# Optimization experiments

Hardware: AMD Instinct MI355X
Metric: run time of the kernel (lower is better)

## Reference

```python
import jax, jax.numpy as jnp
import numpy as np

N = 100000      # n_entities + n_users (graph nodes)
E = 1600000     # edges
R = 8           # relations
D = 64          # entity_dim
DR = 64         # relation_dim
EPS = 1e-12


def setup_inputs() -> dict:
    key = jax.random.key(0)
    ks = jax.random.split(key, 16)
    inp = {
        'entity_emb': jax.random.normal(ks[0], (N, D), jnp.float32) * 0.1,
        'rel_emb':    jax.random.normal(ks[1], (R, DR), jnp.float32) * 0.1,
        'W_R':        jax.random.normal(ks[2], (R, D, DR), jnp.float32) * 0.1,
        'W1_0': jax.random.normal(ks[3], (32, 64), jnp.float32) * 0.1,
        'b1_0': jax.random.normal(ks[4], (32,), jnp.float32) * 0.1,
        'W2_0': jax.random.normal(ks[5], (32, 64), jnp.float32) * 0.1,
        'b2_0': jax.random.normal(ks[6], (32,), jnp.float32) * 0.1,
        'W1_1': jax.random.normal(ks[7], (16, 32), jnp.float32) * 0.1,
        'b1_1': jax.random.normal(ks[8], (16,), jnp.float32) * 0.1,
        'W2_1': jax.random.normal(ks[9], (16, 32), jnp.float32) * 0.1,
        'b2_1': jax.random.normal(ks[10], (16,), jnp.float32) * 0.1,
        'src':   jax.random.randint(ks[11], (E,), 0, N, dtype=jnp.int32),
        'dst':   jax.random.randint(ks[12], (E,), 0, N, dtype=jnp.int32),
        'etype': jax.random.randint(ks[13], (E,), 0, R, dtype=jnp.int32),
    }
    return inp


def _l2_normalize(x):
    # F.normalize(x, p=2, dim=1)
    n = jnp.linalg.norm(x, axis=1, keepdims=True)
    return x / jnp.maximum(n, EPS)


def reference(entity_emb, rel_emb, W_R, W1_0, b1_0, W2_0, b2_0,
              W1_1, b1_1, W2_1, b2_1, src, dst, etype):
    # ---- compute_attention: per-edge relation-specific projection ----
    # proj[n, r, :] = entity_emb[n] @ W_R[r]   -> [N, R, DR]
    proj = jnp.einsum('nd,rdk->nrk', entity_emb, W_R)
    r_mul_t = proj[src, etype]          # [E, DR] (edges.src)
    r_mul_h = proj[dst, etype]          # [E, DR] (edges.dst)
    r_e = rel_emb[etype]                # [E, DR]
    att = jnp.sum(r_mul_t * jnp.tanh(r_mul_h + r_e), axis=-1)  # [E]

    # ---- edge_softmax: normalize over incoming edges of each dst ----
    m = jax.ops.segment_max(att, dst, num_segments=N)           # [N]
    ex = jnp.exp(att - m[dst])
    s = jax.ops.segment_sum(ex, dst, num_segments=N)            # [N]
    a = ex / s[dst]                                             # [E]

    # ---- bi-interaction aggregator layers ----
    def agg_layer(x, W1, b1, W2, b2):
        msg = x[src] * a[:, None]                               # u_mul_e
        Nh = jax.ops.segment_sum(msg, dst, num_segments=N)      # sum to dst
        out1 = jax.nn.leaky_relu(jnp.matmul(x + Nh, W1.T) + b1, 0.01)
        out2 = jax.nn.leaky_relu(jnp.matmul(x * Nh, W2.T) + b2, 0.01)
        return _l2_normalize(out1 + out2)

    ego = entity_emb
    h1 = agg_layer(ego, W1_0, b1_0, W2_0, b2_0)   # [N, 32]
    h2 = agg_layer(h1, W1_1, b1_1, W2_1, b2_1)    # [N, 16]
    all_embed = jnp.concatenate([ego, h1, h2], axis=1)  # [N, 112]
    return all_embed
```

## Files before the change

kernel.cpp:

```cpp
#include <hip/hip_runtime.h>
#include <hip/hip_bf16.h>
#include <math.h>

#define NN 100000
#define NE 1600000
#define NR 8
#define DD 64
#define DDR 64

typedef __attribute__((ext_vector_type(8))) short bf8v;
typedef __attribute__((ext_vector_type(4))) float f4v;

__device__ __forceinline__ unsigned enc_f(float f) {
    unsigned u = __float_as_uint(f);
    return (u & 0x80000000u) ? ~u : (u | 0x80000000u);
}
__device__ __forceinline__ float dec_f(unsigned u) {
    return (u & 0x80000000u) ? __uint_as_float(u & 0x7FFFFFFFu) : __uint_as_float(~u);
}
__device__ __forceinline__ float bflo(unsigned u) { return __uint_as_float(u << 16); }
__device__ __forceinline__ float bfhi(unsigned u) { return __uint_as_float(u & 0xFFFF0000u); }
__device__ __forceinline__ float bfs2f(unsigned short u) { return __uint_as_float(((unsigned)u) << 16); }
__device__ __forceinline__ short f2bfs(float x) {
    __hip_bfloat16 h = __float2bfloat16(x);
    return *reinterpret_cast<short*>(&h);
}
__device__ __forceinline__ unsigned pack2bf(short a, short b) {
    return (unsigned)(unsigned short)a | ((unsigned)(unsigned short)b << 16);
}
__device__ __forceinline__ float tanh_fast(float x) {
    x = fminf(fmaxf(x, -15.f), 15.f);
    float e = __expf(2.f * x);
    return (e - 1.f) * __builtin_amdgcn_rcpf(e + 1.f);
}

__global__ void __launch_bounds__(256)
k_projf(const float* __restrict__ emb, const float* __restrict__ WR,
        const float* __restrict__ rel,
        unsigned short* __restrict__ w2h, unsigned* __restrict__ embh)
{
    __shared__ unsigned short Tt[128][66];
    int t = threadIdx.x;
    int wv = t >> 6, l = t & 63;
    int lo = l & 15, hi = l >> 4;
    int r = blockIdx.y;
    int colbase = (wv & 1) * 32;
    int p = wv >> 1;
    int nwbase = blockIdx.x * 128 + p * 64;
    int nlocal = p * 64;

    const float* __restrict__ wb = WR + (long)r * (DD * DDR) + (hi * 8) * DDR + colbase + lo;
    {
        bf8v B00, B01, B10, B11;
#pragma unroll
        for (int j = 0; j < 8; ++j) {
            B00[j] = f2bfs(wb[(0 * 32 + j) * DDR + 0]);
            B01[j] = f2bfs(wb[(1 * 32 + j) * DDR + 0]);
            B10[j] = f2bfs(wb[(0 * 32 + j) * DDR + 16]);
            B11[j] = f2bfs(wb[(1 * 32 + j) * DDR + 16]);
        }
        float rv0 = rel[r * DDR + colbase + lo];
        float rv1 = rel[r * DDR + colbase + lo + 16];

        for (int nt = 0; nt < 4; ++nt) {
            int nb = nwbase + nt * 16;
            int arow = nb + lo;
            float4 xa0 = make_float4(0.f, 0.f, 0.f, 0.f), xa1 = xa0, xb0 = xa0, xb1 = xa0;
            if (arow < NN) {
                const float* __restrict__ xr = emb + (long)arow * DD + hi * 8;
                xa0 = *(const float4*)(xr);
                xa1 = *(const float4*)(xr + 4);
                xb0 = *(const float4*)(xr + 32);
                xb1 = *(const float4*)(xr + 36);
            }
            bf8v A0, A1;
            A0[0] = f2bfs(xa0.x); A0[1] = f2bfs(xa0.y); A0[2] = f2bfs(xa0.z); A0[3] = f2bfs(xa0.w);
            A0[4] = f2bfs(xa1.x); A0[5] = f2bfs(xa1.y); A0[6] = f2bfs(xa1.z); A0[7] = f2bfs(xa1.w);
            A1[0] = f2bfs(xb0.x); A1[1] = f2bfs(xb0.y); A1[2] = f2bfs(xb0.z); A1[3] = f2bfs(xb0.w);
            A1[4] = f2bfs(xb1.x); A1[5] = f2bfs(xb1.y); A1[6] = f2bfs(xb1.z); A1[7] = f2bfs(xb1.w);

            if (r == 0 && arow < NN) {
                unsigned* er = embh + (long)arow * 32 + hi * 4;
                er[0]  = pack2bf(A0[0], A0[1]); er[1]  = pack2bf(A0[2], A0[3]);
                er[2]  = pack2bf(A0[4], A0[5]); er[3]  = pack2bf(A0[6], A0[7]);
                er[16] = pack2bf(A1[0], A1[1]); er[17] = pack2bf(A1[2], A1[3]);
                er[18] = pack2bf(A1[4], A1[5]); er[19] = pack2bf(A1[6], A1[7]);
            }

            f4v acc0 = {0.f, 0.f, 0.f, 0.f}, acc1 = {0.f, 0.f, 0.f, 0.f};
            acc0 = __builtin_amdgcn_mfma_f32_16x16x32_bf16(A0, B00, acc0, 0, 0, 0);
            acc0 = __builtin_amdgcn_mfma_f32_16x16x32_bf16(A1, B01, acc0, 0, 0, 0);
            acc1 = __builtin_amdgcn_mfma_f32_16x16x32_bf16(A0, B10, acc1, 0, 0, 0);
            acc1 = __builtin_amdgcn_mfma_f32_16x16x32_bf16(A1, B11, acc1, 0, 0, 0);

#pragma unroll
            for (int i = 0; i < 4; ++i) {
                int rl = nlocal + nt * 16 + hi * 4 + i;
                Tt[rl][colbase + lo]      = (unsigned short)f2bfs(tanh_fast(acc0[i] + rv0));
                Tt[rl][colbase + lo + 16] = (unsigned short)f2bfs(tanh_fast(acc1[i] + rv1));
            }
        }
    }
    __syncthreads();

    const float* __restrict__ wb0 = WR + (long)r * (DD * DDR) + (long)(colbase + lo) * DDR + hi * 8;
    const float* __restrict__ wb1 = wb0 + 16 * DDR;
    bf8v C00, C01, C10, C11;
#pragma unroll
    for (int j = 0; j < 8; ++j) {
        C00[j] = f2bfs(wb0[j]);
        C01[j] = f2bfs(wb0[32 + j]);
        C10[j] = f2bfs(wb1[j]);
        C11[j] = f2bfs(wb1[32 + j]);
    }
    for (int nt = 0; nt < 4; ++nt) {
        int nb = nwbase + nt * 16;
        int rl = nlocal + nt * 16 + lo;
        bf8v A0 = *(const bf8v*)&Tt[rl][hi * 8];
        bf8v A1 = *(const bf8v*)&Tt[rl][32 + hi * 8];
        f4v acc0 = {0.f, 0.f, 0.f, 0.f}, acc1 = {0.f, 0.f, 0.f, 0.f};
        acc0 = __builtin_amdgcn_mfma_f32_16x16x32_bf16(A0, C00, acc0, 0, 0, 0);
        acc0 = __builtin_amdgcn_mfma_f32_16x16x32_bf16(A1, C01, acc0, 0, 0, 0);
        acc1 = __builtin_amdgcn_mfma_f32_16x16x32_bf16(A0, C10, acc1, 0, 0, 0);
        acc1 = __builtin_amdgcn_mfma_f32_16x16x32_bf16(A1, C11, acc1, 0, 0, 0);
#pragma unroll
        for (int i = 0; i < 4; ++i) {
            int rr = nb + hi * 4 + i;
            if (rr < NN) {
                long obase = ((long)r * NN + rr) * DDR + colbase + lo;
                w2h[obase]      = (unsigned short)f2bfs(acc0[i]);
                w2h[obase + 16] = (unsigned short)f2bfs(acc1[i]);
            }
        }
    }
}

__global__ void k_hist(const int* __restrict__ dst, unsigned* __restrict__ cnt)
{
    int e = blockIdx.x * blockDim.x + threadIdx.x;
    if (e >= NE) return;
    atomicAdd(cnt + dst[e], 1u);
}

__global__ void k_base(const unsigned* __restrict__ cnt, unsigned* __restrict__ gcur,
                       unsigned* __restrict__ base, unsigned* __restrict__ curs)
{
    int i = blockIdx.x * blockDim.x + threadIdx.x;
    int lane = threadIdx.x & 63;
    unsigned v = (i < NN) ? cnt[i] : 0u;
    unsigned p = v;
#pragma unroll
    for (int off = 1; off < 64; off <<= 1) {
        unsigned q = __shfl_up(p, off);
        if (lane >= off) p += q;
    }
    unsigned tot = __shfl(p, 63);
    unsigned gb = 0;
    if (lane == 0) gb = atomicAdd(gcur, tot);
    gb = __shfl(gb, 0);
    if (i < NN) {
        unsigned b = gb + p - v;
        base[i] = b;
        curs[i] = b;
    }
}

__global__ void k_scatter2(const int* __restrict__ dst, const int* __restrict__ src,
                           const int* __restrict__ et, unsigned* __restrict__ curs,
                           unsigned* __restrict__ srcet)
{
    int e = blockIdx.x * blockDim.x + threadIdx.x;
    if (e >= NE) return;
    unsigned pos = atomicAdd(curs + dst[e], 1u);
    srcet[pos] = (unsigned)src[e] | ((unsigned)et[e] << 28);
}

__global__ void __launch_bounds__(256)
k_mega0(const float* __restrict__ emb, const unsigned* __restrict__ embh,
        const unsigned* __restrict__ w2h,
        const unsigned* __restrict__ cnt, const unsigned* __restrict__ basep,
        const unsigned* __restrict__ srcet, float* __restrict__ acsr,
        unsigned short* __restrict__ h1h,
        const float* __restrict__ W1, const float* __restrict__ b1,
        const float* __restrict__ W2, const float* __restrict__ b2,
        float* __restrict__ out)
{
    __shared__ float W1T[64][33];
    __shared__ float W2T[64][33];
    __shared__ float sm1[4][64];
    __shared__ float sm2[4][64];
    int t = threadIdx.x;
#pragma unroll
    for (int i = 0; i < 8; ++i) {
        int idx = i * 256 + t;
        W1T[idx & 63][idx >> 6] = W1[idx];
        W2T[idx & 63][idx >> 6] = W2[idx];
    }
    int wv = t >> 6, lane = t & 63;
    int g = blockIdx.x * 4 + wv;
    int deg = (int)cnt[g];
    long b = basep[g];
    float Nh = 0.f;
    const unsigned short* embh_us = (const unsigned short*)embh;
    if (deg > 0 && deg <= 64) {
        unsigned se = 0;
        if (lane < deg) se = srcet[b + lane];
        int gi = lane >> 4;
        int lj = lane & 15;
        float acc = 0.f, s_ = 0.f, myexp = 0.f;
        for (int k0 = 0; k0 < deg; k0 += 4) {
            int ei = k0 + gi;
            unsigned sei = __shfl(se, ei);
            int s = (int)(sei & 0x0FFFFFFFu);
            int r = (int)(sei >> 28);
            uint2 tv = *(const uint2*)(embh + (long)s * 32 + lj * 2);
            uint2 hv = *(const uint2*)(w2h + ((long)r * NN + g) * 32 + lj * 2);
            float sum = bflo(tv.x) * bflo(hv.x) + bfhi(tv.x) * bfhi(hv.x)
                      + bflo(tv.y) * bflo(hv.y) + bfhi(tv.y) * bfhi(hv.y);
#pragma unroll
            for (int off = 8; off; off >>= 1) sum += __shfl_xor(sum, off);
#pragma unroll
            for (int q = 0; q < 4; ++q) {
                float sq = __shfl(sum, q * 16);
                float exq = (k0 + q < deg) ? __expf(fminf(sq, 60.f)) : 0.f;
                if (lane == k0 + q) myexp = exq;
                s_ += exq;
                int srcl = q * 16 + (lane >> 2);
                unsigned rx = __shfl(tv.x, srcl);
                unsigned ry = __shfl(tv.y, srcl);
                unsigned word = (lane & 2) ? ry : rx;
                float v = (lane & 1) ? bfhi(word) : bflo(word);
                acc = fmaf(v, exq, acc);
            }
        }
        float inv = 1.f / s_;
        if (lane < deg) acsr[b + lane] = myexp * inv;
        Nh = acc * inv;
    } else if (deg > 64) {
        float m = -3.4e38f;
        for (int i = 0; i < deg; ++i) {
            unsigned sei = srcet[b + i];
            int s = (int)(sei & 0x0FFFFFFFu), r = (int)(sei >> 28);
            float v = bfs2f(embh_us[(long)s * DD + lane]);
            float wvl = bfs2f(((const unsigned short*)w2h)[((long)r * NN + g) * DDR + lane]);
            float p = v * wvl;
#pragma unroll
            for (int off = 32; off; off >>= 1) p += __shfl_xor(p, off);
            if (lane == 0) acsr[b + i] = p;
            m = fmaxf(m, p);
        }
        float s_ = 0.f;
        for (int i = lane; i < deg; i += 64) s_ += __expf(acsr[b + i] - m);
#pragma unroll
        for (int off = 32; off; off >>= 1) s_ += __shfl_xor(s_, off);
        float inv = 1.f / s_;
        float acc = 0.f;
        for (int i = 0; i < deg; ++i) {
            float raw = acsr[b + i];
            float a = __expf(raw - m) * inv;
            int s = (int)(srcet[b + i] & 0x0FFFFFFFu);
            acc = fmaf(bfs2f(embh_us[(long)s * DD + lane]), a, acc);
            if (lane == 0) acsr[b + i] = a;
        }
        Nh = acc;
    }
    float x = emb[(long)g * DD + lane];
    sm1[wv][lane] = x + Nh;
    sm2[wv][lane] = x * Nh;
    __syncthreads();
    int j = lane & 31;
    const float* __restrict__ WT = (lane < 32) ? &W1T[0][0] : &W2T[0][0];
    const float* __restrict__ sm = (lane < 32) ? &sm1[wv][0] : &sm2[wv][0];
    float accm = (lane < 32) ? b1[j] : b2[j];
#pragma unroll 8
    for (int dd = 0; dd < 64; ++dd)
        accm = fmaf(sm[dd], WT[dd * 33 + j], accm);
    accm = (accm >= 0.f) ? accm : 0.01f * accm;
    float other = __shfl_down(accm, 32);
    float h = accm + other;
    float ss = h * h;
#pragma unroll
    for (int off = 16; off; off >>= 1) ss += __shfl_xor(ss, off);
    float hn = h / fmaxf(sqrtf(ss), 1e-12f);
    out[(long)g * 112 + lane] = x;
    if (lane < 32) {
        out[(long)g * 112 + 64 + j] = hn;
        h1h[(long)g * 32 + j] = (unsigned short)f2bfs(hn);
    }
}

__global__ void __launch_bounds__(256)
k_mega1(const float* __restrict__ acsr, const unsigned* __restrict__ srcet,
        const unsigned* __restrict__ cnt, const unsigned* __restrict__ basep,
        const unsigned short* __restrict__ h1h,
        const float* __restrict__ W1, const float* __restrict__ b1,
        const float* __restrict__ W2, const float* __restrict__ b2,
        float* __restrict__ out)
{
    __shared__ float W1T[32][17];
    __shared__ float W2T[32][17];
    __shared__ float sm1[8][32];
    __shared__ float sm2[8][32];
    int t = threadIdx.x;
#pragma unroll
    for (int i = 0; i < 2; ++i) {
        int idx = i * 256 + t;
        W1T[idx & 31][idx >> 5] = W1[idx];
        W2T[idx & 31][idx >> 5] = W2[idx];
    }
    int grp = t >> 5, l5 = t & 31;
    int g = blockIdx.x * 8 + grp;
    int deg = (int)cnt[g];
    float acc = 0.f;
    if (deg > 0) {
        long b = basep[g];
        unsigned se = 0; float a = 0.f;
        if (l5 < deg) { se = srcet[b + l5]; a = acsr[b + l5]; }
        int dmin = (deg < 32) ? deg : 32;
        int i = 0;
        for (; i + 1 < dmin; i += 2) {
            float a0 = __shfl(a, i, 32), a1 = __shfl(a, i + 1, 32);
            int s0 = (int)(__shfl(se, i, 32) & 0x0FFFFFFFu);
            int s1 = (int)(__shfl(se, i + 1, 32) & 0x0FFFFFFFu);
            float v0 = bfs2f(h1h[(long)s0 * 32 + l5]);
            float v1 = bfs2f(h1h[(long)s1 * 32 + l5]);
            acc = fmaf(v0, a0, acc);
            acc = fmaf(v1, a1, acc);
        }
        if (i < dmin) {
            float a0 = __shfl(a, i, 32);
            int s0 = (int)(__shfl(se, i, 32) & 0x0FFFFFFFu);
            acc = fmaf(bfs2f(h1h[(long)s0 * 32 + l5]), a0, acc);
        }
        for (int k = 32; k < deg; ++k) {
            float ak = acsr[b + k];
            int sk = (int)(srcet[b + k] & 0x0FFFFFFFu);
            acc = fmaf(bfs2f(h1h[(long)sk * 32 + l5]), ak, acc);
        }
    }
    float x = out[(long)g * 112 + 64 + l5];
    sm1[grp][l5] = x + acc;
    sm2[grp][l5] = x * acc;
    __syncthreads();
    int j = l5 & 15;
    const float* __restrict__ WT = (l5 < 16) ? &W1T[0][0] : &W2T[0][0];
    const float* __restrict__ sm = (l5 < 16) ? &sm1[grp][0] : &sm2[grp][0];
    float accm = (l5 < 16) ? b1[j] : b2[j];
#pragma unroll 8
    for (int dd = 0; dd < 32; ++dd)
        accm = fmaf(sm[dd], WT[dd * 17 + j], accm);
    accm = (accm >= 0.f) ? accm : 0.01f * accm;
    float other = __shfl_down(accm, 16, 32);
    float h = accm + other;
    float ss = h * h;
#pragma unroll
    for (int off = 8; off; off >>= 1) ss += __shfl_xor(ss, off);
    float hn = h / fmaxf(sqrtf(ss), 1e-12f);
    if (l5 < 16) out[(long)g * 112 + 96 + j] = hn;
}

__global__ void k_att(const float* __restrict__ emb, const float* __restrict__ rel,
                      const float* __restrict__ WR, const int* __restrict__ src,
                      const int* __restrict__ dst, const int* __restrict__ et,
                      float* __restrict__ att, unsigned* __restrict__ mkey)
{
    int e = (int)((blockIdx.x * blockDim.x + threadIdx.x) >> 6);
    int lane = threadIdx.x & 63;
    if (e >= NE) return;
    int s = src[e], d = dst[e], r = et[e];
    const float* __restrict__ es = emb + (long)s * DD;
    const float* __restrict__ eh = emb + (long)d * DD;
    const float* __restrict__ w  = WR + r * (DD * DDR) + lane;
    float at = 0.f, ah = 0.f;
#pragma unroll 8
    for (int dd = 0; dd < DD; ++dd) {
        float ws = w[dd * DDR];
        at = fmaf(es[dd], ws, at);
        ah = fmaf(eh[dd], ws, ah);
    }
    float term = at * tanhf(ah + rel[r * DDR + lane]);
#pragma unroll
    for (int off = 32; off; off >>= 1) term += __shfl_xor(term, off);
    if (lane == 0) {
        att[e] = term;
        atomicMax(mkey + d, enc_f(term));
    }
}

__global__ void k_expsum(const int* __restrict__ dst, float* __restrict__ att,
                         const unsigned* __restrict__ mkey, float* __restrict__ ssum)
{
    int e = blockIdx.x * blockDim.x + threadIdx.x;
    if (e >= NE) return;
    int d = dst[e];
    float ex = expf(att[e] - dec_f(mkey[d]));
    att[e] = ex;
    atomicAdd(ssum + d, ex);
}

__global__ void k_agg0(const float* __restrict__ emb, const int* __restrict__ src,
                       const int* __restrict__ dst, float* __restrict__ att,
                       const float* __restrict__ ssum, float* __restrict__ Nh)
{
    int e = (int)((blockIdx.x * blockDim.x + threadIdx.x) >> 6);
    int lane = threadIdx.x & 63;
    if (e >= NE) return;
    int s = src[e], d = dst[e];
    float a = att[e] / ssum[d];
    if (lane == 0) att[e] = a;
    float v = emb[(long)s * DD + lane] * a;
    atomicAdd(Nh + (long)d * DD + lane, v);
}

__global__ void k_agg1(const float* __restrict__ out, const int* __restrict__ src,
                       const int* __restrict__ dst, const float* __restrict__ att,
                       float* __restrict__ Nh1)
{
    int idx = blockIdx.x * blockDim.x + threadIdx.x;
    int e = idx >> 5;
    int j = idx & 31;
    if (e >= NE) return;
    int s = src[e], d = dst[e];
    float a = att[e];
    float v = out[(long)s * 112 + 64 + j] * a;
    atomicAdd(Nh1 + (long)d * 32 + j, v);
}

#define NPB0 32
__global__ void __launch_bounds__(256)
k_node0t(const float* __restrict__ emb, const float* __restrict__ Nh,
         const float* __restrict__ W1, const float* __restrict__ b1,
         const float* __restrict__ W2, const float* __restrict__ b2,
         float* __restrict__ out)
{
    __shared__ float W1T[64][33];
    __shared__ float W2T[64][33];
    int t = threadIdx.x;
#pragma unroll
    for (int i = 0; i < 8; ++i) {
        int idx = i * 256 + t;
        W1T[idx & 63][idx >> 6] = W1[idx];
        W2T[idx & 63][idx >> 6] = W2[idx];
    }
    __syncthreads();
    int wv = t >> 6, lane = t & 63, j = lane & 31;
    const float* __restrict__ WT = (lane < 32) ? &W1T[0][0] : &W2T[0][0];
    float bj = (lane < 32) ? b1[j] : b2[j];
    int n0 = blockIdx.x * NPB0;
    int n1 = (n0 + NPB0 < NN) ? n0 + NPB0 : NN;
    for (int node = n0 + wv; node < n1; node += 4) {
        const float* __restrict__ x  = emb + (long)node * DD;
        const float* __restrict__ nh = Nh + (long)node * DD;
        float acc = 0.f;
#pragma unroll 8
        for (int dd = 0; dd < DD; ++dd) {
            float xv = x[dd], nv = nh[dd];
            float v = (lane < 32) ? (xv + nv) : (xv * nv);
            acc = fmaf(v, WT[dd * 33 + j], acc);
        }
        acc += bj;
        acc = (acc >= 0.f) ? acc : 0.01f * acc;
        float other = __shfl_down(acc, 32);
        float h = acc + other;
        float ss = h * h;
#pragma unroll
        for (int off = 16; off; off >>= 1) ss += __shfl_xor(ss, off);
        float hn = h / fmaxf(sqrtf(ss), 1e-12f);
        out[(long)node * 112 + lane] = x[lane];
        if (lane < 32) out[(long)node * 112 + 64 + j] = hn;
    }
}

#define NPB1 32
__global__ void __launch_bounds__(256)
k_node1t(const float* __restrict__ outbuf, const float* __restrict__ Nh1,
         const float* __restrict__ W1, const float* __restrict__ b1,
         const float* __restrict__ W2, const float* __restrict__ b2,
         float* __restrict__ out)
{
    __shared__ float W1T[32][17];
    __shared__ float W2T[32][17];
    int t = threadIdx.x;
#pragma unroll
    for (int i = 0; i < 2; ++i) {
        int idx = i * 256 + t;
        W1T[idx & 31][idx >> 5] = W1[idx];
        W2T[idx & 31][idx >> 5] = W2[idx];
    }
    __syncthreads();
    int grp = t >> 5;
    int l5 = t & 31, j = l5 & 15;
    const float* __restrict__ WT = (l5 < 16) ? &W1T[0][0] : &W2T[0][0];
    float bj = (l5 < 16) ? b1[j] : b2[j];
    int n0 = blockIdx.x * NPB1;
    int n1 = (n0 + NPB1 < NN) ? n0 + NPB1 : NN;
    for (int node = n0 + grp; node < n1; node += 8) {
        const float* __restrict__ x  = outbuf + (long)node * 112 + 64;
        const float* __restrict__ nh = Nh1 + (long)node * 32;
        float acc = 0.f;
#pragma unroll 8
        for (int dd = 0; dd < 32; ++dd) {
            float xv = x[dd], nv = nh[dd];
            float v = (l5 < 16) ? (xv + nv) : (xv * nv);
            acc = fmaf(v, WT[dd * 17 + j], acc);
        }
        acc += bj;
        acc = (acc >= 0.f) ? acc : 0.01f * acc;
        float other = __shfl_down(acc, 16, 32);
        float h = acc + other;
        float ss = h * h;
#pragma unroll
        for (int off = 8; off; off >>= 1) ss += __shfl_xor(ss, off);
        float hn = h / fmaxf(sqrtf(ss), 1e-12f);
        if (l5 < 16) out[(long)node * 112 + 96 + j] = hn;
    }
}

extern "C" void kernel_launch(void* const* d_in, const int* in_sizes, int n_in,
                              void* d_out, int out_size, void* d_ws, size_t ws_size,
                              hipStream_t stream) {
    const float* emb  = (const float*)d_in[0];
    const float* rel  = (const float*)d_in[1];
    const float* WR   = (const float*)d_in[2];
    const float* W1_0 = (const float*)d_in[3];
    const float* b1_0 = (const float*)d_in[4];
    const float* W2_0 = (const float*)d_in[5];
    const float* b2_0 = (const float*)d_in[6];
    const float* W1_1 = (const float*)d_in[7];
    const float* b1_1 = (const float*)d_in[8];
    const float* W2_1 = (const float*)d_in[9];
    const float* b2_1 = (const float*)d_in[10];
    const int*   src  = (const int*)d_in[11];
    const int*   dst  = (const int*)d_in[12];
    const int*   et   = (const int*)d_in[13];
    float* out = (float*)d_out;

    unsigned* cnt   = (unsigned*)d_ws;
    unsigned* gcur  = cnt + NN;
    unsigned* basep = cnt + NN + 64;
    unsigned* curs  = cnt + 2 * NN + 64;
    float* acsr  = (float*)d_ws + 3 * NN + 64;
    unsigned* srcet = (unsigned*)(acsr + NE);
    unsigned short* w2h = (unsigned short*)(srcet + NE);
    unsigned* embh = (unsigned*)(w2h + (size_t)NR * NN * DDR);
    unsigned short* h1h = (unsigned short*)(embh + (size_t)NN * 32);

    size_t need = ((size_t)3 * NN + 64 + 2 * (size_t)NE) * 4
                + (size_t)NR * NN * DDR * 2
                + (size_t)NN * 32 * 4 + (size_t)NN * 16 * 4;

    if (ws_size >= need) {
        hipMemsetAsync(d_ws, 0, (size_t)(NN + 64) * sizeof(unsigned), stream);
        k_hist<<<dim3((NE + 255) / 256), dim3(256), 0, stream>>>(dst, cnt);
        k_projf<<<dim3((NN + 127) / 128, NR), dim3(256), 0, stream>>>(
            emb, WR, rel, w2h, embh);
        k_base<<<dim3((NN + 255) / 256), dim3(256), 0, stream>>>(cnt, gcur, basep, curs);
        k_scatter2<<<dim3((NE + 255) / 256), dim3(256), 0, stream>>>(
            dst, src, et, curs, srcet);
        k_mega0<<<dim3((NN + 3) / 4), dim3(256), 0, stream>>>(
            emb, embh, (const unsigned*)w2h, cnt, basep, srcet, acsr, h1h,
            W1_0, b1_0, W2_0, b2_0, out);
        k_mega1<<<dim3((NN + 7) / 8), dim3(256), 0, stream>>>(
            acsr, srcet, cnt, basep, h1h, W1_1, b1_1, W2_1, b2_1, out);
    } else {
        unsigned* mkey = (unsigned*)d_ws;
        float* ssum = (float*)d_ws + NN;
        float* fNh0 = (float*)d_ws + 2 * NN;
        float* fNh1 = (float*)d_ws + (2 + DD) * NN;
        float* fatt = (float*)d_ws + (2 + DD + 32) * NN;
        hipMemsetAsync(d_ws, 0, (size_t)(2 + DD + 32) * NN * sizeof(float), stream);
        k_att<<<dim3((int)(((long)NE * 64 + 255) / 256)), dim3(256), 0, stream>>>(
            emb, rel, WR, src, dst, et, fatt, mkey);
        k_expsum<<<dim3((NE + 255) / 256), dim3(256), 0, stream>>>(dst, fatt, mkey, ssum);
        k_agg0<<<dim3((int)(((long)NE * 64 + 255) / 256)), dim3(256), 0, stream>>>(
            emb, src, dst, fatt, ssum, fNh0);
        k_node0t<<<dim3((NN + NPB0 - 1) / NPB0), dim3(256), 0, stream>>>(
            emb, fNh0, W1_0, b1_0, W2_0, b2_0, out);
        k_agg1<<<dim3((int)(((long)NE * 32 + 255) / 256)), dim3(256), 0, stream>>>(
            out, src, dst, fatt, fNh1);
        k_node1t<<<dim3((NN + NPB1 - 1) / NPB1), dim3(256), 0, stream>>>(
            out, fNh1, W1_1, b1_1, W2_1, b2_1, out);
    }
}
```

Before: 484.6 us.

## Loop over relations inside projection kernel to reuse loaded embedding rows

The projection kernel now gives each block 64 nodes and loops over all 8 relations inside the block, instead of launching one block per (128-node tile, relation). Each embedding row is loaded from global memory and converted to bf16 once, then reused for every relation, rather than being reread 8 times. The trade-off is that W_R is reloaded for every relation in every block, and two block-wide barriers are added per relation. The grid drops from 782x8 blocks to 1563, so each block does more sequential work.

After: 498.7 us. 2.9% more time.

```diff
diff --git a/kernel.cpp b/kernel.cpp
--- a/kernel.cpp
+++ b/kernel.cpp
@@ -35,103 +35,108 @@
 }
 
 __global__ void __launch_bounds__(256)
-k_projf(const float* __restrict__ emb, const float* __restrict__ WR,
-        const float* __restrict__ rel,
-        unsigned short* __restrict__ w2h, unsigned* __restrict__ embh)
-{
-    __shared__ unsigned short Tt[128][66];
+k_projf2(const float* __restrict__ emb, const float* __restrict__ WR,
+         const float* __restrict__ rel,
+         unsigned short* __restrict__ w2h, unsigned* __restrict__ embh)
+{
+    __shared__ unsigned short Tt[64][66];
     int t = threadIdx.x;
     int wv = t >> 6, l = t & 63;
     int lo = l & 15, hi = l >> 4;
-    int r = blockIdx.y;
-    int colbase = (wv & 1) * 32;
+    int q = wv & 1;
     int p = wv >> 1;
-    int nwbase = blockIdx.x * 128 + p * 64;
-    int nlocal = p * 64;
-
-    const float* __restrict__ wb = WR + (long)r * (DD * DDR) + (hi * 8) * DDR + colbase + lo;
-    {
-        bf8v B00, B01, B10, B11;
-#pragma unroll
-        for (int j = 0; j < 8; ++j) {
-            B00[j] = f2bfs(wb[(0 * 32 + j) * DDR + 0]);
-            B01[j] = f2bfs(wb[(1 * 32 + j) * DDR + 0]);
-            B10[j] = f2bfs(wb[(0 * 32 + j) * DDR + 16]);
-            B11[j] = f2bfs(wb[(1 * 32 + j) * DDR + 16]);
-        }
-        float rv0 = rel[r * DDR + colbase + lo];
-        float rv1 = rel[r * DDR + colbase + lo + 16];
-
-        for (int nt = 0; nt < 4; ++nt) {
-            int nb = nwbase + nt * 16;
-            int arow = nb + lo;
-            float4 xa0 = make_float4(0.f, 0.f, 0.f, 0.f), xa1 = xa0, xb0 = xa0, xb1 = xa0;
-            if (arow < NN) {
-                const float* __restrict__ xr = emb + (long)arow * DD + hi * 8;
-                xa0 = *(const float4*)(xr);
-                xa1 = *(const float4*)(xr + 4);
-                xb0 = *(const float4*)(xr + 32);
-                xb1 = *(const float4*)(xr + 36);
+    int colbase = q * 32;
+    int nwbase = blockIdx.x * 64 + p * 32;
+    int nlocal = p * 32;
+
+    bf8v A0[2], A1[2];
+#pragma unroll
+    for (int nt = 0; nt < 2; ++nt) {
+        int arow = nwbase + nt * 16 + lo;
+        float4 xa0 = make_float4(0.f, 0.f, 0.f, 0.f), xa1 = xa0, xb0 = xa0, xb1 = xa0;
+        if (arow < NN) {
+            const float* __restrict__ xr = emb + (long)arow * DD + hi * 8;
+            xa0 = *(const float4*)(xr);
+            xa1 = *(const float4*)(xr + 4);
+            xb0 = *(const float4*)(xr + 32);
+            xb1 = *(const float4*)(xr + 36);
+        }
+        A0[nt][0] = f2bfs(xa0.x); A0[nt][1] = f2bfs(xa0.y); A0[nt][2] = f2bfs(xa0.z); A0[nt][3] = f2bfs(xa0.w);
+        A0[nt][4] = f2bfs(xa1.x); A0[nt][5] = f2bfs(xa1.y); A0[nt][6] = f2bfs(xa1.z); A0[nt][7] = f2bfs(xa1.w);
+        A1[nt][0] = f2bfs(xb0.x); A1[nt][1] = f2bfs(xb0.y); A1[nt][2] = f2bfs(xb0.z); A1[nt][3] = f2bfs(xb0.w);
+        A1[nt][4] = f2bfs(xb1.x); A1[nt][5] = f2bfs(xb1.y); A1[nt][6] = f2bfs(xb1.z); A1[nt][7] = f2bfs(xb1.w);
+        if (q == 0 && arow < NN) {
+            unsigned* er = embh + (long)arow * 32 + hi * 4;
+            er[0]  = pack2bf(A0[nt][0], A0[nt][1]); er[1]  = pack2bf(A0[nt][2], A0[nt][3]);
+            er[2]  = pack2bf(A0[nt][4], A0[nt][5]); er[3]  = pack2bf(A0[nt][6], A0[nt][7]);
+            er[16] = pack2bf(A1[nt][0], A1[nt][1]); er[17] = pack2bf(A1[nt][2], A1[nt][3]);
+            er[18] = pack2bf(A1[nt][4], A1[nt][5]); er[19] = pack2bf(A1[nt][6], A1[nt][7]);
+        }
+    }
+
+    for (int r = 0; r < NR; ++r) {
+        {
+            const float* __restrict__ wb = WR + (long)r * (DD * DDR) + (hi * 8) * DDR + colbase + lo;
+            bf8v B00, B01, B10, B11;
+#pragma unroll
+            for (int j = 0; j < 8; ++j) {
+                B00[j] = f2bfs(wb[(0 * 32 + j) * DDR + 0]);
+                B01[j] = f2bfs(wb[(1 * 32 + j) * DDR + 0]);
+                B10[j] = f2bfs(wb[(0 * 32 + j) * DDR + 16]);
+                B11[j] = f2bfs(wb[(1 * 32 + j) * DDR + 16]);
             }
-            bf8v A0, A1;
-            A0[0] = f2bfs(xa0.x); A0[1] = f2bfs(xa0.y); A0[2] = f2bfs(xa0.z); A0[3] = f2bfs(xa0.w);
-            A0[4] = f2bfs(xa1.x); A0[5] = f2bfs(xa1.y); A0[6] = f2bfs(xa1.z); A0[7] = f2bfs(xa1.w);
-            A1[0] = f2bfs(xb0.x); A1[1] = f2bfs(xb0.y); A1[2] = f2bfs(xb0.z); A1[3] = f2bfs(xb0.w);
-            A1[4] = f2bfs(xb1.x); A1[5] = f2bfs(xb1.y); A1[6] = f2bfs(xb1.z); A1[7] = f2bfs(xb1.w);
-
-            if (r == 0 && arow < NN) {
-                unsigned* er = embh + (long)arow * 32 + hi * 4;
-                er[0]  = pack2bf(A0[0], A0[1]); er[1]  = pack2bf(A0[2], A0[3]);
-                er[2]  = pack2bf(A0[4], A0[5]); er[3]  = pack2bf(A0[6], A0[7]);
-                er[16] = pack2bf(A1[0], A1[1]); er[17] = pack2bf(A1[2], A1[3]);
-                er[18] = pack2bf(A1[4], A1[5]); er[19] = pack2bf(A1[6], A1[7]);
+            float rv0 = rel[r * DDR + colbase + lo];
+            float rv1 = rel[r * DDR + colbase + lo + 16];
+#pragma unroll
+            for (int nt = 0; nt < 2; ++nt) {
+                f4v acc0 = {0.f, 0.f, 0.f, 0.f}, acc1 = {0.f, 0.f, 0.f, 0.f};
+                acc0 = __builtin_amdgcn_mfma_f32_16x16x32_bf16(A0[nt], B00, acc0, 0, 0, 0);
+                acc0 = __builtin_amdgcn_mfma_f32_16x16x32_bf16(A1[nt], B01, acc0, 0, 0, 0);
+                acc1 = __builtin_amdgcn_mfma_f32_16x16x32_bf16(A0[nt], B10, acc1, 0, 0, 0);
+                acc1 = __builtin_amdgcn_mfma_f32_16x16x32_bf16(A1[nt], B11, acc1, 0, 0, 0);
+#pragma unroll
+                for (int i = 0; i < 4; ++i) {
+                    int rl = nlocal + nt * 16 + hi * 4 + i;
+                    Tt[rl][colbase + lo]      = (unsigned short)f2bfs(tanh_fast(acc0[i] + rv0));
+                    Tt[rl][colbase + lo + 16] = (unsigned short)f2bfs(tanh_fast(acc1[i] + rv1));
+                }
             }
-
-            f4v acc0 = {0.f, 0.f, 0.f, 0.f}, acc1 = {0.f, 0.f, 0.f, 0.f};
-            acc0 = __builtin_amdgcn_mfma_f32_16x16x32_bf16(A0, B00, acc0, 0, 0, 0);
-            acc0 = __builtin_amdgcn_mfma_f32_16x16x32_bf16(A1, B01, acc0, 0, 0, 0);
-            acc1 = __builtin_amdgcn_mfma_f32_16x16x32_bf16(A0, B10, acc1, 0, 0, 0);
-            acc1 = __builtin_amdgcn_mfma_f32_16x16x32_bf16(A1, B11, acc1, 0, 0, 0);
-
-#pragma unroll
-            for (int i = 0; i < 4; ++i) {
-                int rl = nlocal + nt * 16 + hi * 4 + i;
-                Tt[rl][colbase + lo]      = (unsigned short)f2bfs(tanh_fast(acc0[i] + rv0));
-                Tt[rl][colbase + lo + 16] = (unsigned short)f2bfs(tanh_fast(acc1[i] + rv1));
+        }
+        __syncthreads();
+        {
+            const float* __restrict__ wb0 = WR + (long)r * (DD * DDR) + (long)(colbase + lo) * DDR + hi * 8;
+            const float* __restrict__ wb1 = wb0 + 16 * DDR;
+            bf8v C00, C01, C10, C11;
+#pragma unroll
+            for (int j = 0; j < 8; ++j) {
+                C00[j] = f2bfs(wb0[j]);
+                C01[j] = f2bfs(wb0[32 + j]);
+                C10[j] = f2bfs(wb1[j]);
+                C11[j] = f2bfs(wb1[32 + j]);
             }
-        }
-    }
-    __syncthreads();
-
-    const float* __restrict__ wb0 = WR + (long)r * (DD * DDR) + (long)(colbase + lo) * DDR + hi * 8;
-    const float* __restrict__ wb1 = wb0 + 16 * DDR;
-    bf8v C00, C01, C10, C11;
-#pragma unroll
-    for (int j = 0; j < 8; ++j) {
-        C00[j] = f2bfs(wb0[j]);
-        C01[j] = f2bfs(wb0[32 + j]);
-        C10[j] = f2bfs(wb1[j]);
-        C11[j] = f2bfs(wb1[32 + j]);
-    }
-    for (int nt = 0; nt < 4; ++nt) {
-        int nb = nwbase + nt * 16;
-        int rl = nlocal + nt * 16 + lo;
-        bf8v A0 = *(const bf8v*)&Tt[rl][hi * 8];
-        bf8v A1 = *(const bf8v*)&Tt[rl][32 + hi * 8];
-        f4v acc0 = {0.f, 0.f, 0.f, 0.f}, acc1 = {0.f, 0.f, 0.f, 0.f};
-        acc0 = __builtin_amdgcn_mfma_f32_16x16x32_bf16(A0, C00, acc0, 0, 0, 0);
-        acc0 = __builtin_amdgcn_mfma_f32_16x16x32_bf16(A1, C01, acc0, 0, 0, 0);
-        acc1 = __builtin_amdgcn_mfma_f32_16x16x32_bf16(A0, C10, acc1, 0, 0, 0);
-        acc1 = __builtin_amdgcn_mfma_f32_16x16x32_bf16(A1, C11, acc1, 0, 0, 0);
-#pragma unroll
-        for (int i = 0; i < 4; ++i) {
-            int rr = nb + hi * 4 + i;
-            if (rr < NN) {
-                long obase = ((long)r * NN + rr) * DDR + colbase + lo;
-                w2h[obase]      = (unsigned short)f2bfs(acc0[i]);
-                w2h[obase + 16] = (unsigned short)f2bfs(acc1[i]);
+#pragma unroll
+            for (int nt = 0; nt < 2; ++nt) {
+                int nb = nwbase + nt * 16;
+                int rl = nlocal + nt * 16 + lo;
+                bf8v T0 = *(const bf8v*)&Tt[rl][hi * 8];
+                bf8v T1 = *(const bf8v*)&Tt[rl][32 + hi * 8];
+                f4v acc0 = {0.f, 0.f, 0.f, 0.f}, acc1 = {0.f, 0.f, 0.f, 0.f};
+                acc0 = __builtin_amdgcn_mfma_f32_16x16x32_bf16(T0, C00, acc0, 0, 0, 0);
+                acc0 = __builtin_amdgcn_mfma_f32_16x16x32_bf16(T1, C01, acc0, 0, 0, 0);
+                acc1 = __builtin_amdgcn_mfma_f32_16x16x32_bf16(T0, C10, acc1, 0, 0, 0);
+                acc1 = __builtin_amdgcn_mfma_f32_16x16x32_bf16(T1, C11, acc1, 0, 0, 0);
+#pragma unroll
+                for (int i = 0; i < 4; ++i) {
+                    int rr = nb + hi * 4 + i;
+                    if (rr < NN) {
+                        long obase = ((long)r * NN + rr) * DDR + colbase + lo;
+                        w2h[obase]      = (unsigned short)f2bfs(acc0[i]);
+                        w2h[obase + 16] = (unsigned short)f2bfs(acc1[i]);
+                    }
+                }
             }
         }
+        __syncthreads();
     }
 }
 
@@ -552,7 +557,7 @@
     if (ws_size >= need) {
         hipMemsetAsync(d_ws, 0, (size_t)(NN + 64) * sizeof(unsigned), stream);
         k_hist<<<dim3((NE + 255) / 256), dim3(256), 0, stream>>>(dst, cnt);
-        k_projf<<<dim3((NN + 127) / 128, NR), dim3(256), 0, stream>>>(
+        k_projf2<<<dim3((NN + 63) / 64), dim3(256), 0, stream>>>(
             emb, WR, rel, w2h, embh);
         k_base<<<dim3((NN + 255) / 256), dim3(256), 0, stream>>>(cnt, gcur, basep, curs);
         k_scatter2<<<dim3((NE + 255) / 256), dim3(256), 0, stream>>>(
```
